# Kernel optimization log

Measured on AMD Instinct MI355X. Metric: run time of the kernel, lower is better.

## Reference

```python
import jax, jax.numpy as jnp
import numpy as np

B, L, D = 4, 2048, 256
MAX_NGRAM = 3
SLOTS = 64


def setup_inputs() -> dict:
    key = jax.random.key(0)
    k1, k2, k3 = jax.random.split(key, 3)
    x = jax.random.normal(k1, (B, L, D), dtype=jnp.float32)
    memory = jax.random.normal(k2, (SLOTS, MAX_NGRAM, D), dtype=jnp.float32)
    pos_bias = jax.random.normal(k3, (SLOTS, MAX_NGRAM), dtype=jnp.float32)
    return {"x": x, "memory": memory, "pos_bias": pos_bias}


def _extract_ngrams(x, max_ngram):
    # Left-pad with max_ngram-1 zero vectors, then take max_ngram shifted views.
    b, l, d = x.shape
    xpad = jnp.concatenate([jnp.zeros((b, max_ngram - 1, d), x.dtype), x], axis=1)
    # ngrams[b, l, n] = xpad[b, n + l]  -> (B, L, N, d)
    return jnp.stack([xpad[:, n:n + l] for n in range(max_ngram)], axis=2)


def reference(x, memory, pos_bias):
    slots, max_ngram, d = memory.shape
    ngrams = _extract_ngrams(x, max_ngram)                      # (B, L, N, d)
    # Contraction over d replaces the huge (B,L,M,N,d) broadcast-multiply.
    sims = jnp.einsum('blnd,mnd->blmn', ngrams, memory)         # (B, L, M, N)
    scores = sims + pos_bias[None, None]                        # (B, L, M, N)
    best = jnp.argmax(scores, axis=-1)                          # (B, L, M) int
    # selected[b,l,m] = memory[m, best[b,l,m]]  -> (B, L, M, d)
    selected = memory[jnp.arange(slots)[None, None, :], best]
    return selected.sum(axis=2)                                 # (B, L, d)
```

## Files before the change

kernel.cpp:

```cpp
#include <hip/hip_runtime.h>
#include <stdint.h>

#define LL   2048
#define DD   256
#define SLOTS 64
#define MN   192
#define PT   8192

typedef _Float16 half8 __attribute__((ext_vector_type(8)));
typedef float    f32x4 __attribute__((ext_vector_type(4)));

#define FRAG_ELEMS (MN * DD)

__global__ __launch_bounds__(256) void prep_kernel(
    const float* __restrict__ mem,
    _Float16* __restrict__ aS_h, _Float16* __restrict__ aS_l,
    _Float16* __restrict__ bG_h)
{
    const int e = blockIdx.x * 256 + threadIdx.x;
    const int mnp = e >> 8;
    const int d   = e & 255;
    const int n = mnp >> 6, m = mnp & 63;
    const float v = mem[((m * 3 + n) << 8) + d];
    const _Float16 h  = (_Float16)v;
    const _Float16 lo = (_Float16)(v - (float)h);

    {
        const int tm = mnp >> 4, r = mnp & 15;
        const int c = d >> 5, q = (d >> 3) & 3, j = d & 7;
        const int i1 = ((tm * 8 + c) * 64 + (q * 16 + r)) * 8 + j;
        aS_h[i1] = h; aS_l[i1] = lo;
    }
    {
        const int c2 = mnp >> 5, q2 = (mnp >> 3) & 3, j2 = mnp & 7;
        const int td = d >> 4, n2 = d & 15;
        const int i2 = ((td * 6 + c2) * 64 + (q2 * 16 + n2)) * 8 + j2;
        bG_h[i2] = h;
    }
}

__global__ __launch_bounds__(512, 4) void fused_kernel(
    const float* __restrict__ x, const float* __restrict__ bias,
    const _Float16* __restrict__ aS_h, const _Float16* __restrict__ aS_l,
    const _Float16* __restrict__ bG_h,
    float* __restrict__ out)
{
    __shared__ __align__(16) _Float16 xfh[2 * 8 * 64 * 8];
    __shared__ __align__(16) _Float16 xfl[2 * 8 * 64 * 8];
    __shared__ float    scores[MN * 19];
    __shared__ float    biasS[MN];
    __shared__ uint32_t selS[16 * 8];

    const int p0   = blockIdx.x * 16;
    const int tid  = threadIdx.x;
    const int lane = tid & 63;
    const int w    = tid >> 6;
    const int q    = lane >> 4, col = lane & 15;
    const int pg   = w >> 2;
    const int tmg  = w & 3;

    half8 ah[2][3], al[2][3];
#pragma unroll
    for (int i = 0; i < 3; ++i) {
        const int tm = tmg * 3 + i;
        const size_t off = (size_t)((tm * 8 + 0) * 64 + lane) * 8;
        ah[0][i] = *(const half8*)(aS_h + off);
        al[0][i] = *(const half8*)(aS_l + off);
    }

    if (tid < MN) {
        const int m = tid & 63, n = tid >> 6;
        biasS[tid] = bias[m * 3 + n];
    }

    {
        const int rr = tid >> 4;
        const int dc = tid & 15;
        int g = p0 - 2 + rr;
        g = g < 0 ? 0 : (g > PT - 1 ? PT - 1 : g);
        const float4* xr = (const float4*)(x + (size_t)g * DD + dc * 16);
        const int pt = rr >> 4, lr = rr & 15;
        const int c  = dc >> 1, h = dc & 1;
#pragma unroll
        for (int s = 0; s < 2; ++s) {
            const float4 u = xr[s * 2];
            const float4 v = xr[s * 2 + 1];
            float f[8] = {u.x, u.y, u.z, u.w, v.x, v.y, v.z, v.w};
            half8 hi, lo;
#pragma unroll
            for (int j = 0; j < 8; ++j) {
                const _Float16 hh = (_Float16)f[j];
                hi[j] = hh;
                lo[j] = (_Float16)(f[j] - (float)hh);
            }
            const int base = ((pt * 8 + c) * 64 + (2 * h + s) * 16 + lr) * 8;
            *(half8*)(xfh + base) = hi;
            *(half8*)(xfl + base) = lo;
        }
    }
    __syncthreads();

    {
        f32x4 acc[3];
#pragma unroll
        for (int i = 0; i < 3; ++i) acc[i] = (f32x4){0.f, 0.f, 0.f, 0.f};

        half8 bh[2], bl[2];
        {
            const int base = ((pg * 8 + 0) * 64 + lane) * 8;
            bh[0] = *(const half8*)(xfh + base);
            bl[0] = *(const half8*)(xfl + base);
        }

#pragma unroll
        for (int c = 0; c < 8; ++c) {
            const int cur = c & 1, nxt = cur ^ 1;
            if (c < 7) {
#pragma unroll
                for (int i = 0; i < 3; ++i) {
                    const int tm = tmg * 3 + i;
                    const size_t off = (size_t)((tm * 8 + c + 1) * 64 + lane) * 8;
                    ah[nxt][i] = *(const half8*)(aS_h + off);
                    al[nxt][i] = *(const half8*)(aS_l + off);
                }
                const int base = ((pg * 8 + c + 1) * 64 + lane) * 8;
                bh[nxt] = *(const half8*)(xfh + base);
                bl[nxt] = *(const half8*)(xfl + base);
            }
#pragma unroll
            for (int i = 0; i < 3; ++i) {
                acc[i] = __builtin_amdgcn_mfma_f32_16x16x32_f16(ah[cur][i], bh[cur], acc[i], 0, 0, 0);
                acc[i] = __builtin_amdgcn_mfma_f32_16x16x32_f16(ah[cur][i], bl[cur], acc[i], 0, 0, 0);
                acc[i] = __builtin_amdgcn_mfma_f32_16x16x32_f16(al[cur][i], bh[cur], acc[i], 0, 0, 0);
            }
        }

        const int wp = pg * 16 + col;
#pragma unroll
        for (int i = 0; i < 3; ++i) {
            const int tm = tmg * 3 + i;
            if (wp < 18) {
#pragma unroll
                for (int r = 0; r < 4; ++r)
                    scores[(tm * 16 + q * 4 + r) * 19 + wp] = acc[i][r];
            }
        }
    }

    half8 mg[2][2];
#pragma unroll
    for (int i = 0; i < 2; ++i) {
        const int td = w * 2 + i;
        const size_t off = (size_t)((td * 6 + 0) * 64 + lane) * 8;
        mg[0][i] = *(const half8*)(bG_h + off);
    }
    __syncthreads();

#pragma unroll
    for (int it = 0; it < 2; ++it) {
        const int pl = w * 2 + it;
        const int m  = lane;
        const int p  = p0 + pl;
        const int l  = p & (LL - 1);
        const float v0 = ((l >= 2) ? scores[(      m) * 19 + pl + 0] : 0.f) + biasS[      m];
        const float v1 = ((l >= 1) ? scores[( 64 + m) * 19 + pl + 1] : 0.f) + biasS[ 64 + m];
        const float v2 =             scores[(128 + m) * 19 + pl + 2]        + biasS[128 + m];
        int bn = 0; float bv = v0;
        if (v1 > bv) { bv = v1; bn = 1; }
        if (v2 > bv) { bv = v2; bn = 2; }
        const unsigned long long b0 = __ballot(bn == 0);
        const unsigned long long b1 = __ballot(bn == 1);
        const unsigned long long b2 = __ballot(bn == 2);
        if (lane < 6) {
            const unsigned long long B = (lane >> 1) == 0 ? b0 : ((lane >> 1) == 1 ? b1 : b2);
            selS[pl * 8 + lane] = (uint32_t)(B >> ((lane & 1) * 32));
        }
    }
    __syncthreads();

    {
        uint32_t sw[6];
#pragma unroll
        for (int c = 0; c < 6; ++c) sw[c] = selS[col * 8 + c];

        f32x4 acc2[2];
#pragma unroll
        for (int i = 0; i < 2; ++i) acc2[i] = (f32x4){0.f, 0.f, 0.f, 0.f};

        const _Float16 ONE = (_Float16)1.f, ZERO = (_Float16)0.f;
        const int qb = q * 8;
#pragma unroll
        for (int c = 0; c < 6; ++c) {
            const int cur = c & 1, nxt = cur ^ 1;
            if (c < 5) {
#pragma unroll
                for (int i = 0; i < 2; ++i) {
                    const int td = w * 2 + i;
                    const size_t off = (size_t)((td * 6 + c + 1) * 64 + lane) * 8;
                    mg[nxt][i] = *(const half8*)(bG_h + off);
                }
            }
            half8 sel;
#pragma unroll
            for (int j = 0; j < 8; ++j)
                sel[j] = ((sw[c] >> (qb + j)) & 1u) ? ONE : ZERO;
#pragma unroll
            for (int i = 0; i < 2; ++i)
                acc2[i] = __builtin_amdgcn_mfma_f32_16x16x32_f16(sel, mg[cur][i], acc2[i], 0, 0, 0);
        }

#pragma unroll
        for (int i = 0; i < 2; ++i) {
            const int td = w * 2 + i;
#pragma unroll
            for (int r = 0; r < 4; ++r)
                out[(size_t)(p0 + q * 4 + r) * DD + td * 16 + col] = acc2[i][r];
        }
    }
}

extern "C" void kernel_launch(void* const* d_in, const int* in_sizes, int n_in,
                              void* d_out, int out_size, void* d_ws, size_t ws_size,
                              hipStream_t stream) {
    (void)in_sizes; (void)n_in; (void)out_size; (void)ws_size;
    const float* x    = (const float*)d_in[0];
    const float* mem  = (const float*)d_in[1];
    const float* bias = (const float*)d_in[2];
    float* out = (float*)d_out;

    _Float16* aS_h = (_Float16*)d_ws;
    _Float16* aS_l = aS_h + FRAG_ELEMS;
    _Float16* bG_h = aS_l + FRAG_ELEMS;

    prep_kernel<<<FRAG_ELEMS / 256, 256, 0, stream>>>(mem, aS_h, aS_l, bG_h);
    fused_kernel<<<PT / 16, 512, 0, stream>>>(x, bias, aS_h, aS_l, bG_h, out);
}
```

Measured before the change: 78.61 us.

## Process 32 positions per block with 12 waves, one memory tile per wave

Doubles the positions handled per block from 16 to 32 and raises the block to 768 threads (12 waves). Each wave now owns one 16-row memory tile and sweeps all three position tiles, so the mem fragments fetched per block from global/L2 are amortized over twice as many positions and the 2-halo overhead shrinks. The gather phase redistributes 32 output tiles across 12 waves. The cost is more shared memory and registers per block, fewer blocks (256) on the GPU, and uneven work in the later phases.

```diff
diff --git a/kernel.cpp b/kernel.cpp
--- a/kernel.cpp
+++ b/kernel.cpp
@@ -39,33 +39,30 @@
     }
 }
 
-__global__ __launch_bounds__(512, 4) void fused_kernel(
+__global__ __launch_bounds__(768, 3) void fused_kernel(
     const float* __restrict__ x, const float* __restrict__ bias,
     const _Float16* __restrict__ aS_h, const _Float16* __restrict__ aS_l,
     const _Float16* __restrict__ bG_h,
     float* __restrict__ out)
 {
-    __shared__ __align__(16) _Float16 xfh[2 * 8 * 64 * 8];
-    __shared__ __align__(16) _Float16 xfl[2 * 8 * 64 * 8];
-    __shared__ float    scores[MN * 19];
+    __shared__ __align__(16) _Float16 xfh[3 * 8 * 64 * 8];
+    __shared__ __align__(16) _Float16 xfl[3 * 8 * 64 * 8];
+    __shared__ float    scores[MN * 35];
     __shared__ float    biasS[MN];
-    __shared__ uint32_t selS[16 * 8];
-
-    const int p0   = blockIdx.x * 16;
+    __shared__ uint32_t selS[32 * 8];
+
+    const int p0   = blockIdx.x * 32;
     const int tid  = threadIdx.x;
     const int lane = tid & 63;
     const int w    = tid >> 6;
     const int q    = lane >> 4, col = lane & 15;
-    const int pg   = w >> 2;
-    const int tmg  = w & 3;
-
-    half8 ah[2][3], al[2][3];
-#pragma unroll
-    for (int i = 0; i < 3; ++i) {
-        const int tm = tmg * 3 + i;
+    const int tm   = w;
+
+    half8 ah[2], al[2];
+    {
         const size_t off = (size_t)((tm * 8 + 0) * 64 + lane) * 8;
-        ah[0][i] = *(const half8*)(aS_h + off);
-        al[0][i] = *(const half8*)(aS_l + off);
+        ah[0] = *(const half8*)(aS_h + off);
+        al[0] = *(const half8*)(aS_l + off);
     }
 
     if (tid < MN) {
@@ -73,98 +70,89 @@
         biasS[tid] = bias[m * 3 + n];
     }
 
-    {
-        const int rr = tid >> 4;
-        const int dc = tid & 15;
+#pragma unroll
+    for (int k = 0; k < 2; ++k) {
+        const int idx = tid + k * 768;
+        const int rr  = idx >> 5;
+        const int ch  = idx & 31;
         int g = p0 - 2 + rr;
         g = g < 0 ? 0 : (g > PT - 1 ? PT - 1 : g);
-        const float4* xr = (const float4*)(x + (size_t)g * DD + dc * 16);
+        const float4* xr = (const float4*)(x + (size_t)g * DD + ch * 8);
+        const float4 u = xr[0];
+        const float4 v = xr[1];
+        float f[8] = {u.x, u.y, u.z, u.w, v.x, v.y, v.z, v.w};
+        half8 hi, lo;
+#pragma unroll
+        for (int j = 0; j < 8; ++j) {
+            const _Float16 hh = (_Float16)f[j];
+            hi[j] = hh;
+            lo[j] = (_Float16)(f[j] - (float)hh);
+        }
+        const int c = ch >> 2, qq = ch & 3;
         const int pt = rr >> 4, lr = rr & 15;
-        const int c  = dc >> 1, h = dc & 1;
-#pragma unroll
-        for (int s = 0; s < 2; ++s) {
-            const float4 u = xr[s * 2];
-            const float4 v = xr[s * 2 + 1];
-            float f[8] = {u.x, u.y, u.z, u.w, v.x, v.y, v.z, v.w};
-            half8 hi, lo;
-#pragma unroll
-            for (int j = 0; j < 8; ++j) {
-                const _Float16 hh = (_Float16)f[j];
-                hi[j] = hh;
-                lo[j] = (_Float16)(f[j] - (float)hh);
-            }
-            const int base = ((pt * 8 + c) * 64 + (2 * h + s) * 16 + lr) * 8;
-            *(half8*)(xfh + base) = hi;
-            *(half8*)(xfl + base) = lo;
-        }
+        const int base = ((pt * 8 + c) * 64 + qq * 16 + lr) * 8;
+        *(half8*)(xfh + base) = hi;
+        *(half8*)(xfl + base) = lo;
     }
     __syncthreads();
 
     {
         f32x4 acc[3];
 #pragma unroll
-        for (int i = 0; i < 3; ++i) acc[i] = (f32x4){0.f, 0.f, 0.f, 0.f};
-
-        half8 bh[2], bl[2];
-        {
-            const int base = ((pg * 8 + 0) * 64 + lane) * 8;
-            bh[0] = *(const half8*)(xfh + base);
-            bl[0] = *(const half8*)(xfl + base);
+        for (int p = 0; p < 3; ++p) acc[p] = (f32x4){0.f, 0.f, 0.f, 0.f};
+
+        half8 bh[2][3], bl[2][3];
+#pragma unroll
+        for (int p = 0; p < 3; ++p) {
+            const int base = ((p * 8 + 0) * 64 + lane) * 8;
+            bh[0][p] = *(const half8*)(xfh + base);
+            bl[0][p] = *(const half8*)(xfl + base);
         }
 
 #pragma unroll
         for (int c = 0; c < 8; ++c) {
             const int cur = c & 1, nxt = cur ^ 1;
             if (c < 7) {
-#pragma unroll
-                for (int i = 0; i < 3; ++i) {
-                    const int tm = tmg * 3 + i;
-                    const size_t off = (size_t)((tm * 8 + c + 1) * 64 + lane) * 8;
-                    ah[nxt][i] = *(const half8*)(aS_h + off);
-                    al[nxt][i] = *(const half8*)(aS_l + off);
+                const size_t off = (size_t)((tm * 8 + c + 1) * 64 + lane) * 8;
+                ah[nxt] = *(const half8*)(aS_h + off);
+                al[nxt] = *(const half8*)(aS_l + off);
+#pragma unroll
+                for (int p = 0; p < 3; ++p) {
+                    const int base = ((p * 8 + c + 1) * 64 + lane) * 8;
+                    bh[nxt][p] = *(const half8*)(xfh + base);
+                    bl[nxt][p] = *(const half8*)(xfl + base);
                 }
-                const int base = ((pg * 8 + c + 1) * 64 + lane) * 8;
-                bh[nxt] = *(const half8*)(xfh + base);
-                bl[nxt] = *(const half8*)(xfl + base);
-            }
-#pragma unroll
-            for (int i = 0; i < 3; ++i) {
-                acc[i] = __builtin_amdgcn_mfma_f32_16x16x32_f16(ah[cur][i], bh[cur], acc[i], 0, 0, 0);
-                acc[i] = __builtin_amdgcn_mfma_f32_16x16x32_f16(ah[cur][i], bl[cur], acc[i], 0, 0, 0);
-                acc[i] = __builtin_amdgcn_mfma_f32_16x16x32_f16(al[cur][i], bh[cur], acc[i], 0, 0, 0);
-            }
-        }
-
-        const int wp = pg * 16 + col;
-#pragma unroll
-        for (int i = 0; i < 3; ++i) {
-            const int tm = tmg * 3 + i;
-            if (wp < 18) {
+            }
+#pragma unroll
+            for (int p = 0; p < 3; ++p) {
+                acc[p] = __builtin_amdgcn_mfma_f32_16x16x32_f16(ah[cur], bh[cur][p], acc[p], 0, 0, 0);
+                acc[p] = __builtin_amdgcn_mfma_f32_16x16x32_f16(ah[cur], bl[cur][p], acc[p], 0, 0, 0);
+                acc[p] = __builtin_amdgcn_mfma_f32_16x16x32_f16(al[cur], bh[cur][p], acc[p], 0, 0, 0);
+            }
+        }
+
+#pragma unroll
+        for (int p = 0; p < 3; ++p) {
+            const int wp = p * 16 + col;
+            if (wp < 34) {
 #pragma unroll
                 for (int r = 0; r < 4; ++r)
-                    scores[(tm * 16 + q * 4 + r) * 19 + wp] = acc[i][r];
-            }
-        }
-    }
-
-    half8 mg[2][2];
-#pragma unroll
-    for (int i = 0; i < 2; ++i) {
-        const int td = w * 2 + i;
-        const size_t off = (size_t)((td * 6 + 0) * 64 + lane) * 8;
-        mg[0][i] = *(const half8*)(bG_h + off);
-    }
+                    scores[(tm * 16 + q * 4 + r) * 35 + wp] = acc[p][r];
+            }
+        }
+    }
+
+    half8 mg[2];
+    mg[0] = *(const half8*)(bG_h + (size_t)((w * 6 + 0) * 64 + lane) * 8);
     __syncthreads();
 
-#pragma unroll
-    for (int it = 0; it < 2; ++it) {
-        const int pl = w * 2 + it;
-        const int m  = lane;
-        const int p  = p0 + pl;
-        const int l  = p & (LL - 1);
-        const float v0 = ((l >= 2) ? scores[(      m) * 19 + pl + 0] : 0.f) + biasS[      m];
-        const float v1 = ((l >= 1) ? scores[( 64 + m) * 19 + pl + 1] : 0.f) + biasS[ 64 + m];
-        const float v2 =             scores[(128 + m) * 19 + pl + 2]        + biasS[128 + m];
+    for (int pl = w; pl < 32; pl += 12) {
+        const int m = lane;
+        const int p = p0 + pl;
+        const int l = p & (LL - 1);
+        const float v0 = ((l >= 2) ? scores[(      m) * 35 + pl + 0] : 0.f) + biasS[      m];
+        const float v1 = ((l >= 1) ? scores[( 64 + m) * 35 + pl + 1] : 0.f) + biasS[ 64 + m];
+        const float v2 =             scores[(128 + m) * 35 + pl + 2]        + biasS[128 + m];
         int bn = 0; float bv = v0;
         if (v1 > bv) { bv = v1; bn = 1; }
         if (v2 > bv) { bv = v2; bn = 2; }
@@ -179,42 +167,41 @@
     __syncthreads();
 
     {
-        uint32_t sw[6];
-#pragma unroll
-        for (int c = 0; c < 6; ++c) sw[c] = selS[col * 8 + c];
-
-        f32x4 acc2[2];
-#pragma unroll
-        for (int i = 0; i < 2; ++i) acc2[i] = (f32x4){0.f, 0.f, 0.f, 0.f};
-
         const _Float16 ONE = (_Float16)1.f, ZERO = (_Float16)0.f;
         const int qb = q * 8;
 #pragma unroll
-        for (int c = 0; c < 6; ++c) {
-            const int cur = c & 1, nxt = cur ^ 1;
-            if (c < 5) {
-#pragma unroll
-                for (int i = 0; i < 2; ++i) {
-                    const int td = w * 2 + i;
-                    const size_t off = (size_t)((td * 6 + c + 1) * 64 + lane) * 8;
-                    mg[nxt][i] = *(const half8*)(bG_h + off);
+        for (int ti = 0; ti < 3; ++ti) {
+            const int t = w + ti * 12;
+            if (t < 32) {
+                const int pt = t >> 4, td = t & 15;
+                uint32_t sw[6];
+#pragma unroll
+                for (int c = 0; c < 6; ++c) sw[c] = selS[(pt * 16 + col) * 8 + c];
+
+                f32x4 acc2 = (f32x4){0.f, 0.f, 0.f, 0.f};
+#pragma unroll
+                for (int c = 0; c < 6; ++c) {
+                    const int cur = c & 1, nxt = cur ^ 1;
+                    if (c < 5) {
+                        mg[nxt] = *(const half8*)(bG_h + (size_t)((td * 6 + c + 1) * 64 + lane) * 8);
+                    } else {
+                        const int tn = t + 12;
+                        if (tn < 32) {
+                            const int tdn = tn & 15;
+                            mg[nxt] = *(const half8*)(bG_h + (size_t)((tdn * 6 + 0) * 64 + lane) * 8);
+                        }
+                    }
+                    half8 sel;
+#pragma unroll
+                    for (int j = 0; j < 8; ++j)
+                        sel[j] = ((sw[c] >> (qb + j)) & 1u) ? ONE : ZERO;
+                    acc2 = __builtin_amdgcn_mfma_f32_16x16x32_f16(sel, mg[cur], acc2, 0, 0, 0);
                 }
-            }
-            half8 sel;
-#pragma unroll
-            for (int j = 0; j < 8; ++j)
-                sel[j] = ((sw[c] >> (qb + j)) & 1u) ? ONE : ZERO;
-#pragma unroll
-            for (int i = 0; i < 2; ++i)
-                acc2[i] = __builtin_amdgcn_mfma_f32_16x16x32_f16(sel, mg[cur][i], acc2[i], 0, 0, 0);
-        }
-
-#pragma unroll
-        for (int i = 0; i < 2; ++i) {
-            const int td = w * 2 + i;
-#pragma unroll
-            for (int r = 0; r < 4; ++r)
-                out[(size_t)(p0 + q * 4 + r) * DD + td * 16 + col] = acc2[i][r];
+
+#pragma unroll
+                for (int r = 0; r < 4; ++r)
+                    out[(size_t)(p0 + pt * 16 + q * 4 + r) * DD + td * 16 + col] = acc2[r];
+            }
         }
     }
 }
@@ -233,5 +220,5 @@
     _Float16* bG_h = aS_l + FRAG_ELEMS;
 
     prep_kernel<<<FRAG_ELEMS / 256, 256, 0, stream>>>(mem, aS_h, aS_l, bG_h);
-    fused_kernel<<<PT / 16, 512, 0, stream>>>(x, bias, aS_h, aS_l, bG_h, out);
+    fused_kernel<<<PT / 32, 768, 0, stream>>>(x, bias, aS_h, aS_l, bG_h, out);
 }
```

New measurement: 73.32 us. 6.7% less time.
